# Optimization experiments

Hardware: AMD Instinct MI355X
Metric: run time of the kernel (lower is better)

The kernel has to match this reference:

```python
import jax, jax.numpy as jnp
import numpy as np

N, E, G = 2048, 4096, 16
IN_DIM, HID, E_DIM, EDGE_H = 11, 128, 6, 64
EPS = 1e-5


def setup_inputs() -> dict:
    key = jax.random.key(0)
    ks = jax.random.split(key, 32)
    s = 0.1  # keep activations tame
    inp = {
        "h": jax.random.normal(ks[0], (N, IN_DIM), jnp.float32),
        "e": jax.random.normal(ks[1], (E, E_DIM), jnp.float32),
        "src": jax.random.randint(ks[2], (E,), 0, N, jnp.int32),
        "dst": jax.random.randint(ks[3], (E,), 0, N, jnp.int32),
        "node_graph": (jnp.arange(N, dtype=jnp.int32) // (N // G)),
        # layer 0 (in_dim=11 -> hid=128)
        "eW1_0": jax.random.normal(ks[4], (E_DIM, EDGE_H), jnp.float32) * s,
        "eb1_0": jax.random.normal(ks[5], (EDGE_H,), jnp.float32) * s,
        "eW2_0": jax.random.normal(ks[6], (EDGE_H, IN_DIM * HID), jnp.float32) * s,
        "eb2_0": jax.random.normal(ks[7], (IN_DIM * HID,), jnp.float32) * s,
        "bias_0": jax.random.normal(ks[8], (HID,), jnp.float32) * s,
        "gamma_0": jax.random.uniform(ks[9], (HID,), jnp.float32, 0.5, 1.5),
        "beta_0": jax.random.normal(ks[10], (HID,), jnp.float32) * s,
        "mean_0": jax.random.normal(ks[11], (HID,), jnp.float32) * s,
        "var_0": jax.random.uniform(ks[12], (HID,), jnp.float32, 0.5, 1.5),
        # layers 1..3 stacked (hid -> hid)
        "eW1": jax.random.normal(ks[13], (3, E_DIM, EDGE_H), jnp.float32) * s,
        "eb1": jax.random.normal(ks[14], (3, EDGE_H), jnp.float32) * s,
        "eW2": jax.random.normal(ks[15], (3, EDGE_H, HID * HID), jnp.float32) * s,
        "eb2": jax.random.normal(ks[16], (3, HID * HID), jnp.float32) * s,
        "bias": jax.random.normal(ks[17], (3, HID), jnp.float32) * s,
        "gamma": jax.random.uniform(ks[18], (3, HID), jnp.float32, 0.5, 1.5),
        "beta": jax.random.normal(ks[19], (3, HID), jnp.float32) * s,
        "mean": jax.random.normal(ks[20], (3, HID), jnp.float32) * s,
        "var": jax.random.uniform(ks[21], (3, HID), jnp.float32, 0.5, 1.5),
        # output BN (on mean readout)
        "g_out": jax.random.uniform(ks[22], (HID,), jnp.float32, 0.5, 1.5),
        "b_out": jax.random.normal(ks[23], (HID,), jnp.float32) * s,
        "m_out": jax.random.normal(ks[24], (HID,), jnp.float32) * s,
        "v_out": jax.random.uniform(ks[25], (HID,), jnp.float32, 0.5, 1.5),
    }
    return inp


def _bn(x, ga, be, mu, vv):
    return (x - mu) * jax.lax.rsqrt(vv + EPS) * ga + be


def _nn_layer(x, e, src, dst, W1, b1, W2, b2, bb, ga, be, mu, vv, din):
    # edge MLP -> per-edge weight matrix [E, din, HID]
    w = (jax.nn.relu(e @ W1 + b1) @ W2 + b2).reshape(E, din, HID)
    msg = jnp.einsum('ei,eio->eo', x[src], w)          # per-edge message [E, HID]
    agg = jax.ops.segment_sum(msg, dst, num_segments=N)
    deg = jax.ops.segment_sum(jnp.ones((E,), x.dtype), dst, num_segments=N)
    agg = agg / jnp.maximum(deg, 1.0)[:, None] + bb    # mean aggregation + NNConv bias
    return _bn(jax.nn.relu(agg), ga, be, mu, vv)       # relu -> BatchNorm (eval)


def reference(h, e, src, dst, node_graph, eW1_0, eb1_0, eW2_0, eb2_0, bias_0,
              gamma_0, beta_0, mean_0, var_0, eW1, eb1, eW2, eb2, bias,
              gamma, beta, mean, var, g_out, b_out, m_out, v_out):
    x = _nn_layer(h, e, src, dst, eW1_0, eb1_0, eW2_0, eb2_0, bias_0,
                  gamma_0, beta_0, mean_0, var_0, IN_DIM)
    for i in range(3):
        x = _nn_layer(x, e, src, dst, eW1[i], eb1[i], eW2[i], eb2[i], bias[i],
                      gamma[i], beta[i], mean[i], var[i], HID)
    # dropout is identity in eval mode
    cnt = jax.ops.segment_sum(jnp.ones((N,), x.dtype), node_graph, num_segments=G)
    hn = jax.ops.segment_sum(x, node_graph, num_segments=G) / cnt[:, None]
    hx = jax.ops.segment_max(x, node_graph, num_segments=G)
    hn = _bn(hn, g_out, b_out, m_out, v_out)
    return jnp.concatenate([hn, hx], axis=1)  # [G, 2*HID]
```

## Files before the change

### kernel.cpp

```cpp
#include <hip/hip_runtime.h>
#include <stdint.h>

#define N_NODES 2048
#define N_EDGES 4096
#define N_GRAPH 16
#define IN_DIM  11
#define HID     128
#define E_DIMF  6
#define EDGE_H  64
#define NSLICE  65
#define ZCOLS   (NSLICE*HID)
#define BN_EPS  1e-5f

typedef __attribute__((ext_vector_type(8))) short short8;
typedef __attribute__((ext_vector_type(4))) float f32x4;

static __device__ __forceinline__ float bf2f(unsigned short u) {
  union { float f; uint32_t i; } x; x.i = ((uint32_t)u) << 16; return x.f;
}
static __device__ __forceinline__ unsigned short f2bf(float f) {
  union { float f; uint32_t i; } x; x.f = f;
  uint32_t i = x.i;
  return (unsigned short)((i + 0x7FFFu + ((i >> 16) & 1u)) >> 16);
}

__global__ void calc_deg_i(const int* __restrict__ dst, int* __restrict__ degi) {
  int e = blockIdx.x * 256 + threadIdx.x;
  if (e < N_EDGES) atomicAdd(&degi[dst[e]], 1);
}

__global__ __launch_bounds__(256) void build_offsets(const int* __restrict__ degi,
                                                     int* __restrict__ roff,
                                                     int* __restrict__ cursor) {
  __shared__ int part[256];
  int t = threadIdx.x;
  int base = t * 8;
  int loc[8];
  int s = 0;
#pragma unroll
  for (int j = 0; j < 8; ++j) { loc[j] = s; s += degi[base + j]; }
  part[t] = s;
  __syncthreads();
  int pre = 0;
  for (int i = 0; i < t; ++i) pre += part[i];
#pragma unroll
  for (int j = 0; j < 8; ++j) {
    int v = pre + loc[j];
    roff[base + j] = v;
    cursor[base + j] = v;
  }
  if (t == 255) roff[N_NODES] = pre + s;
}

__global__ void scatter_edges(const int* __restrict__ dst, int* __restrict__ cursor,
                              int* __restrict__ elist) {
  int e = blockIdx.x * 256 + threadIdx.x;
  if (e < N_EDGES) {
    int pos = atomicAdd(&cursor[dst[e]], 1);
    elist[pos] = e;
  }
}

__global__ __launch_bounds__(256) void prep(const float* __restrict__ W2_0,
                                            const float* __restrict__ b2_0,
                                            const float* __restrict__ W2L,
                                            const float* __restrict__ b2L,
                                            const float* __restrict__ h_in,
                                            unsigned short* __restrict__ WbT0,
                                            unsigned short* __restrict__ WbTL,
                                            unsigned short* __restrict__ xb0) {
  const int y = blockIdx.y, t = threadIdx.x;
  if (y == 4) {
    for (int idx = blockIdx.x * 256 + t; idx < N_NODES * 32; idx += 65 * 256) {
      int n = idx >> 5, i = idx & 31;
      xb0[idx] = f2bf(i < IN_DIM ? h_in[n * IN_DIM + i] : 0.0f);
    }
    return;
  }
  __shared__ unsigned short tile[128 * 130];
  const int k = blockIdx.x;
  if (y == 0) {
    const float* src = (k < 64) ? (W2_0 + (size_t)k * IN_DIM * HID) : b2_0;
    for (int j = t; j < IN_DIM * HID; j += 256) {
      int i = j >> 7, o = j & 127;
      tile[i * 130 + o] = f2bf(src[j]);
    }
    __syncthreads();
    for (int j = t; j < HID * 32; j += 256) {
      int o = j >> 5, i = j & 31;
      WbT0[((size_t)k * HID + o) * 32 + i] =
          (i < IN_DIM) ? tile[i * 130 + o] : (unsigned short)0;
    }
  } else {
    const int l = y - 1;
    const float* src = (k < 64) ? (W2L + ((size_t)l * 64 + k) * (HID * HID))
                                : (b2L + (size_t)l * (HID * HID));
    unsigned short* dstp = WbTL + (size_t)l * ZCOLS * HID;
    for (int j = t; j < HID * HID; j += 256) {
      int i = j >> 7, o = j & 127;
      tile[i * 130 + o] = f2bf(src[j]);
    }
    __syncthreads();
    for (int j = t; j < HID * HID; j += 256) {
      int o = j >> 7, i = j & 127;
      dstp[((size_t)k * HID + o) * HID + i] = tile[i * 130 + o];
    }
  }
}

template <int KP, int SWZ>
__global__ __launch_bounds__(256) void gemm_z(const unsigned short* __restrict__ Xb,
                                              const unsigned short* __restrict__ WbT,
                                              unsigned short* __restrict__ Z) {
  extern __shared__ unsigned short lds[];
  unsigned short* Al = lds;
  unsigned short* Bl = lds + 128 * KP;
  const int nb = blockIdx.x;
  const int mb = blockIdx.y;
  const int t = threadIdx.x;
  const int ROWB = KP * 2;
  const int NCH = 128 * ROWB / 16;
  const unsigned short* Asrc = Xb + (size_t)mb * 128 * KP;
  const unsigned short* Bsrc = WbT + (size_t)nb * 128 * KP;
  for (int c = t; c < NCH; c += 256) {
    int off = c * 16;
    int row = off / ROWB;
    int kb = off % ROWB;
    int dsto = row * ROWB + (kb ^ ((row & SWZ) << 4));
    *(uint4*)((char*)Al + dsto) = *(const uint4*)((const char*)Asrc + off);
    *(uint4*)((char*)Bl + dsto) = *(const uint4*)((const char*)Bsrc + off);
  }
  __syncthreads();

  const int w = t >> 6, l = t & 63;
  const int wm = (w >> 1) * 64, wn = (w & 1) * 64;
  const int lr = l & 15, lh = l >> 4;
  f32x4 acc[4][4] = {};
#pragma unroll
  for (int kk = 0; kk < KP; kk += 32) {
    short8 a[4], b[4];
    const int kb = (kk + lh * 8) * 2;
#pragma unroll
    for (int mi = 0; mi < 4; ++mi) {
      int row = wm + mi * 16 + lr;
      int addr = row * ROWB + (kb ^ ((row & SWZ) << 4));
      a[mi] = *(const short8*)((const char*)Al + addr);
    }
#pragma unroll
    for (int ni = 0; ni < 4; ++ni) {
      int col = wn + ni * 16 + lr;
      int addr = col * ROWB + (kb ^ ((col & SWZ) << 4));
      b[ni] = *(const short8*)((const char*)Bl + addr);
    }
#pragma unroll
    for (int mi = 0; mi < 4; ++mi)
#pragma unroll
      for (int ni = 0; ni < 4; ++ni)
        acc[mi][ni] = __builtin_amdgcn_mfma_f32_16x16x32_bf16(b[ni], a[mi], acc[mi][ni], 0, 0, 0);
  }
#pragma unroll
  for (int mi = 0; mi < 4; ++mi) {
    const int node = mb * 128 + wm + mi * 16 + lr;
    unsigned short* zp = Z + (size_t)node * ZCOLS + nb * 128 + wn + lh * 4;
#pragma unroll
    for (int ni = 0; ni < 4; ++ni) {
      ushort4 pk;
      pk.x = f2bf(acc[mi][ni][0]);
      pk.y = f2bf(acc[mi][ni][1]);
      pk.z = f2bf(acc[mi][ni][2]);
      pk.w = f2bf(acc[mi][ni][3]);
      *(ushort4*)(zp + ni * 16) = pk;
    }
  }
}

template <int LAST>
__global__ __launch_bounds__(128) void node_gather(
    const float* __restrict__ efeat, const float* __restrict__ W1,
    const float* __restrict__ b1, const unsigned short* __restrict__ Z,
    const int* __restrict__ elist, const int* __restrict__ roff,
    const int* __restrict__ src,
    const float* __restrict__ bias, const float* __restrict__ gamma,
    const float* __restrict__ beta, const float* __restrict__ mean,
    const float* __restrict__ var,
    unsigned short* __restrict__ xbout,
    const int* __restrict__ ng, float* __restrict__ gsum,
    unsigned int* __restrict__ gmax, float* __restrict__ gcnt) {
  const int n = blockIdx.x, t = threadIdx.x;
  const int cg = t & 15, kg = t >> 4;
  const int start = roff[n], end = roff[n + 1];
  __shared__ float hs[EDGE_H];
  __shared__ float red[128][9];
  float acc8[8] = {};
  for (int idx = start; idx < end; ++idx) {
    const int e = elist[idx];
    __syncthreads();
    if (t < EDGE_H) {
      float a = b1[t];
#pragma unroll
      for (int j = 0; j < E_DIMF; ++j) a += efeat[e * E_DIMF + j] * W1[j * EDGE_H + t];
      hs[t] = fmaxf(a, 0.f);
    }
    __syncthreads();
    const unsigned short* zr = Z + (size_t)src[e] * ZCOLS + cg * 8;
#pragma unroll
    for (int kk = 0; kk < 8; ++kk) {
      const int k = kg * 8 + kk;
      short8 v = *(const short8*)(zr + k * HID);
      const float hk = hs[k];
#pragma unroll
      for (int j = 0; j < 8; ++j) acc8[j] += hk * bf2f((unsigned short)v[j]);
    }
    if (kg == 0) {
      short8 v = *(const short8*)(zr + 64 * HID);
#pragma unroll
      for (int j = 0; j < 8; ++j) acc8[j] += bf2f((unsigned short)v[j]);
    }
  }
#pragma unroll
  for (int j = 0; j < 8; ++j) red[t][j] = acc8[j];
  __syncthreads();
  const int o = t;
  float s = 0.f;
#pragma unroll
  for (int k2 = 0; k2 < 8; ++k2) s += red[k2 * 16 + (o >> 3)][o & 7];
  const int dg = end - start;
  float v = s / (float)(dg > 0 ? dg : 1) + bias[o];
  v = fmaxf(v, 0.f);
  v = (v - mean[o]) * rsqrtf(var[o] + BN_EPS) * gamma[o] + beta[o];
  if (!LAST) {
    xbout[n * HID + o] = f2bf(v);
  } else {
    const int g = ng[n];
    atomicAdd(&gsum[g * HID + o], v);
    unsigned int u = __float_as_uint(v);
    unsigned int key = (u & 0x80000000u) ? ~u : (u | 0x80000000u);
    atomicMax(&gmax[g * HID + o], key);
    if (o == 0) atomicAdd(&gcnt[g], 1.f);
  }
}

__global__ void out_final(const float* __restrict__ gsum, const unsigned int* __restrict__ gmax,
                          const float* __restrict__ gcnt,
                          const float* __restrict__ g_out, const float* __restrict__ b_out,
                          const float* __restrict__ m_out, const float* __restrict__ v_out,
                          float* __restrict__ out) {
  int g = blockIdx.x, t = threadIdx.x;
  float hn = gsum[g * HID + t] / fmaxf(gcnt[g], 1.0f);
  hn = (hn - m_out[t]) * rsqrtf(v_out[t] + BN_EPS) * g_out[t] + b_out[t];
  unsigned int key = gmax[g * HID + t];
  unsigned int u = (key & 0x80000000u) ? (key ^ 0x80000000u) : ~key;
  out[g * 2 * HID + t] = hn;
  out[g * 2 * HID + HID + t] = __uint_as_float(u);
}

extern "C" void kernel_launch(void* const* d_in, const int* in_sizes, int n_in,
                              void* d_out, int out_size, void* d_ws, size_t ws_size,
                              hipStream_t stream) {
  const float* h_in   = (const float*)d_in[0];
  const float* e_in   = (const float*)d_in[1];
  const int*   src    = (const int*)d_in[2];
  const int*   dst    = (const int*)d_in[3];
  const int*   ng     = (const int*)d_in[4];
  const float* eW1_0  = (const float*)d_in[5];
  const float* eb1_0  = (const float*)d_in[6];
  const float* eW2_0  = (const float*)d_in[7];
  const float* eb2_0  = (const float*)d_in[8];
  const float* bias_0 = (const float*)d_in[9];
  const float* gamma_0= (const float*)d_in[10];
  const float* beta_0 = (const float*)d_in[11];
  const float* mean_0 = (const float*)d_in[12];
  const float* var_0  = (const float*)d_in[13];
  const float* eW1    = (const float*)d_in[14];
  const float* eb1    = (const float*)d_in[15];
  const float* eW2    = (const float*)d_in[16];
  const float* eb2    = (const float*)d_in[17];
  const float* biasL  = (const float*)d_in[18];
  const float* gammaL = (const float*)d_in[19];
  const float* betaL  = (const float*)d_in[20];
  const float* meanL  = (const float*)d_in[21];
  const float* varL   = (const float*)d_in[22];
  const float* g_out  = (const float*)d_in[23];
  const float* b_out  = (const float*)d_in[24];
  const float* m_out  = (const float*)d_in[25];
  const float* v_out  = (const float*)d_in[26];
  float* out = (float*)d_out;

  char* ws = (char*)d_ws;
  size_t off = 0;
  auto alloc = [&](size_t bytes) {
    void* p = ws + off;
    off = (off + bytes + 255) & ~(size_t)255;
    return p;
  };
  unsigned short* Z    = (unsigned short*)alloc((size_t)N_NODES * ZCOLS * 2);
  unsigned short* WbT0 = (unsigned short*)alloc((size_t)ZCOLS * 32 * 2);
  unsigned short* WbTL = (unsigned short*)alloc((size_t)3 * ZCOLS * HID * 2);
  unsigned short* xb0  = (unsigned short*)alloc((size_t)N_NODES * 32 * 2);
  unsigned short* xb   = (unsigned short*)alloc((size_t)N_NODES * HID * 2);
  float* gsum          = (float*)alloc((size_t)N_GRAPH * HID * 4);
  unsigned int* gmax   = (unsigned int*)alloc((size_t)N_GRAPH * HID * 4);
  float* gcnt          = (float*)alloc((size_t)N_GRAPH * 4);
  int*   degi          = (int*)alloc((size_t)N_NODES * 4);
  size_t zbytes = (size_t)((char*)(degi + N_NODES) - (char*)gsum);
  int* roff            = (int*)alloc((size_t)(N_NODES + 1) * 4);
  int* cursor          = (int*)alloc((size_t)N_NODES * 4);
  int* elist           = (int*)alloc((size_t)N_EDGES * 4);

  hipMemsetAsync(gsum, 0, zbytes, stream);
  calc_deg_i<<<N_EDGES / 256, 256, 0, stream>>>(dst, degi);
  build_offsets<<<1, 256, 0, stream>>>(degi, roff, cursor);
  scatter_edges<<<N_EDGES / 256, 256, 0, stream>>>(dst, cursor, elist);
  prep<<<dim3(65, 5), 256, 0, stream>>>(eW2_0, eb2_0, eW2, eb2, h_in, WbT0, WbTL, xb0);

  gemm_z<32, 3><<<dim3(65, 16), 256, 2 * 128 * 32 * 2, stream>>>(xb0, WbT0, Z);
  node_gather<0><<<N_NODES, 128, 0, stream>>>(e_in, eW1_0, eb1_0, Z, elist, roff, src,
                                              bias_0, gamma_0, beta_0, mean_0, var_0,
                                              xb, ng, gsum, gmax, gcnt);

  for (int l = 0; l < 3; ++l) {
    gemm_z<128, 7><<<dim3(65, 16), 256, 2 * 128 * 128 * 2, stream>>>(
        xb, WbTL + (size_t)l * ZCOLS * HID, Z);
    if (l < 2) {
      node_gather<0><<<N_NODES, 128, 0, stream>>>(
          e_in, eW1 + l * E_DIMF * EDGE_H, eb1 + l * EDGE_H, Z, elist, roff, src,
          biasL + l * HID, gammaL + l * HID, betaL + l * HID, meanL + l * HID,
          varL + l * HID, xb, ng, gsum, gmax, gcnt);
    } else {
      node_gather<1><<<N_NODES, 128, 0, stream>>>(
          e_in, eW1 + l * E_DIMF * EDGE_H, eb1 + l * EDGE_H, Z, elist, roff, src,
          biasL + l * HID, gammaL + l * HID, betaL + l * HID, meanL + l * HID,
          varL + l * HID, xb, ng, gsum, gmax, gcnt);
    }
  }

  out_final<<<N_GRAPH, HID, 0, stream>>>(gsum, gmax, gcnt, g_out, b_out, m_out, v_out, out);
}
```

Baseline: 203.0 us.

## Fuse whole pipeline into one cooperative persistent kernel with grid syncs

Replaces the sequence of about a dozen launches (degree count, offsets, scatter, weight transpose, GEMMs, gathers, readout) with one cooperative kernel of 256 blocks by 512 threads that separates phases with grid-wide syncs. It also reworks the gather so each block handles four nodes at once and every thread computes the edge MLP hidden values itself, removing the per-edge LDS broadcast and its block barriers. The aim is to cut launch overhead and inter-kernel gaps. In exchange, the GEMM and transpose now run as persistent loops on a fixed grid, which may lower occupancy and parallelism, and every phase boundary pays a grid barrier. The old multi-launch path stays as a fallback when cooperative launch is unavailable.

```diff
diff --git a/kernel.cpp b/kernel.cpp
--- a/kernel.cpp
+++ b/kernel.cpp
@@ -1,5 +1,8 @@
 #include <hip/hip_runtime.h>
+#include <hip/hip_cooperative_groups.h>
 #include <stdint.h>
+
+namespace cg = cooperative_groups;
 
 #define N_NODES 2048
 #define N_EDGES 4096
@@ -11,6 +14,8 @@
 #define NSLICE  65
 #define ZCOLS   (NSLICE*HID)
 #define BN_EPS  1e-5f
+#define MEGA_BLOCKS 256
+#define MEGA_THREADS 512
 
 typedef __attribute__((ext_vector_type(8))) short short8;
 typedef __attribute__((ext_vector_type(4))) float f32x4;
@@ -23,6 +28,286 @@
   uint32_t i = x.i;
   return (unsigned short)((i + 0x7FFFu + ((i >> 16) & 1u)) >> 16);
 }
+
+struct MegaP {
+  const float *h_in, *e_in;
+  const int *src, *dst, *ng;
+  const float *eW1_0, *eb1_0, *eW2_0, *eb2_0;
+  const float *bias_0, *gamma_0, *beta_0, *mean_0, *var_0;
+  const float *eW1, *eb1, *eW2, *eb2;
+  const float *biasL, *gammaL, *betaL, *meanL, *varL;
+  const float *g_out, *b_out, *m_out, *v_out;
+  float *out;
+  unsigned short *Z, *WbT0, *WbTL, *xb0, *xb;
+  float *gsum;
+  unsigned int *gmax;
+  float *gcnt;
+  int *roff, *cursor, *elist;
+};
+
+
+static __device__ void transpose_slab(const MegaP& p, int s, char* smem) {
+  unsigned short* tile = (unsigned short*)smem;
+  const int t = threadIdx.x;
+  if (s < 65) {
+    const int k = s;
+    const float* srcp = (k < 64) ? (p.eW2_0 + (size_t)k * IN_DIM * HID) : p.eb2_0;
+    for (int j = t; j < IN_DIM * HID; j += MEGA_THREADS) {
+      int i = j >> 7, o = j & 127;
+      tile[i * 130 + o] = f2bf(srcp[j]);
+    }
+    __syncthreads();
+    for (int j = t; j < HID * 32; j += MEGA_THREADS) {
+      int o = j >> 5, i = j & 31;
+      p.WbT0[((size_t)k * HID + o) * 32 + i] =
+          (i < IN_DIM) ? tile[i * 130 + o] : (unsigned short)0;
+    }
+    __syncthreads();
+  } else {
+    const int sl = s - 65, l = sl / 65, k = sl % 65;
+    const float* srcp = (k < 64) ? (p.eW2 + ((size_t)l * 64 + k) * (HID * HID))
+                                 : (p.eb2 + (size_t)l * (HID * HID));
+    unsigned short* dstp = p.WbTL + (size_t)l * ZCOLS * HID;
+    for (int j = t; j < HID * HID; j += MEGA_THREADS) {
+      int i = j >> 7, o = j & 127;
+      tile[i * 130 + o] = f2bf(srcp[j]);
+    }
+    __syncthreads();
+    for (int j = t; j < HID * HID; j += MEGA_THREADS) {
+      int o = j >> 7, i = j & 127;
+      dstp[((size_t)k * HID + o) * HID + i] = tile[i * 130 + o];
+    }
+    __syncthreads();
+  }
+}
+
+template <int KP, int SWZ>
+static __device__ void gemm_phase(const unsigned short* Xb, const unsigned short* WbT,
+                                  unsigned short* Z, char* smem) {
+  unsigned short* Al = (unsigned short*)smem;
+  unsigned short* Bl = Al + 128 * KP;
+  const int t = threadIdx.x;
+  const int ROWB = KP * 2;
+  const int NCH = 128 * ROWB / 16;
+  const int w = t >> 6, l = t & 63;
+  const int wm = (w >> 2) * 64, wn = (w & 3) * 32;
+  const int lr = l & 15, lh = l >> 4;
+  for (int tile = blockIdx.x; tile < 65 * 16; tile += gridDim.x) {
+    const int nb = tile % 65, mb = tile / 65;
+    const unsigned short* Asrc = Xb + (size_t)mb * 128 * KP;
+    const unsigned short* Bsrc = WbT + (size_t)nb * 128 * KP;
+    for (int c = t; c < NCH; c += MEGA_THREADS) {
+      int off = c * 16;
+      int row = off / ROWB;
+      int kb = off % ROWB;
+      int dsto = row * ROWB + (kb ^ ((row & SWZ) << 4));
+      *(uint4*)((char*)Al + dsto) = *(const uint4*)((const char*)Asrc + off);
+      *(uint4*)((char*)Bl + dsto) = *(const uint4*)((const char*)Bsrc + off);
+    }
+    __syncthreads();
+    f32x4 acc[4][2] = {};
+#pragma unroll
+    for (int kk = 0; kk < KP; kk += 32) {
+      short8 a[4], b[2];
+      const int kb = (kk + lh * 8) * 2;
+#pragma unroll
+      for (int mi = 0; mi < 4; ++mi) {
+        int row = wm + mi * 16 + lr;
+        int addr = row * ROWB + (kb ^ ((row & SWZ) << 4));
+        a[mi] = *(const short8*)((const char*)Al + addr);
+      }
+#pragma unroll
+      for (int ni = 0; ni < 2; ++ni) {
+        int col = wn + ni * 16 + lr;
+        int addr = col * ROWB + (kb ^ ((col & SWZ) << 4));
+        b[ni] = *(const short8*)((const char*)Bl + addr);
+      }
+#pragma unroll
+      for (int mi = 0; mi < 4; ++mi)
+#pragma unroll
+        for (int ni = 0; ni < 2; ++ni)
+          acc[mi][ni] = __builtin_amdgcn_mfma_f32_16x16x32_bf16(b[ni], a[mi], acc[mi][ni], 0, 0, 0);
+    }
+#pragma unroll
+    for (int mi = 0; mi < 4; ++mi) {
+      const int node = mb * 128 + wm + mi * 16 + lr;
+      unsigned short* zp = Z + (size_t)node * ZCOLS + nb * 128 + wn + lh * 4;
+#pragma unroll
+      for (int ni = 0; ni < 2; ++ni) {
+        ushort4 pk;
+        pk.x = f2bf(acc[mi][ni][0]);
+        pk.y = f2bf(acc[mi][ni][1]);
+        pk.z = f2bf(acc[mi][ni][2]);
+        pk.w = f2bf(acc[mi][ni][3]);
+        *(ushort4*)(zp + ni * 16) = pk;
+      }
+    }
+    __syncthreads();
+  }
+}
+
+template <int LAST>
+static __device__ void gather_phase(const MegaP& p, const float* W1, const float* b1,
+                                    const float* bias, const float* gamma,
+                                    const float* beta, const float* mean,
+                                    const float* var, char* smem) {
+  float* red = (float*)smem;
+  const int t = threadIdx.x;
+  const int hh = t >> 7, tt = t & 127;
+  const int cgi = tt & 15, kg = tt >> 4;
+  for (int n0 = blockIdx.x * 4; n0 < N_NODES; n0 += gridDim.x * 4) {
+    const int n = n0 + hh;
+    const int start = p.roff[n], end = p.roff[n + 1];
+    float acc8[8] = {};
+    for (int idx = start; idx < end; ++idx) {
+      const int e = p.elist[idx];
+      float ef[E_DIMF];
+#pragma unroll
+      for (int j = 0; j < E_DIMF; ++j) ef[j] = p.e_in[e * E_DIMF + j];
+      float hk[8];
+#pragma unroll
+      for (int kk = 0; kk < 8; ++kk) {
+        const int k = kg * 8 + kk;
+        float a = b1[k];
+#pragma unroll
+        for (int j = 0; j < E_DIMF; ++j) a += ef[j] * W1[j * EDGE_H + k];
+        hk[kk] = fmaxf(a, 0.f);
+      }
+      const unsigned short* zr = p.Z + (size_t)p.src[e] * ZCOLS + cgi * 8;
+#pragma unroll
+      for (int kk = 0; kk < 8; ++kk) {
+        short8 v = *(const short8*)(zr + (kg * 8 + kk) * HID);
+        const float hv = hk[kk];
+#pragma unroll
+        for (int j = 0; j < 8; ++j) acc8[j] += hv * bf2f((unsigned short)v[j]);
+      }
+      if (kg == 0) {
+        short8 v = *(const short8*)(zr + 64 * HID);
+#pragma unroll
+        for (int j = 0; j < 8; ++j) acc8[j] += bf2f((unsigned short)v[j]);
+      }
+    }
+    __syncthreads();
+#pragma unroll
+    for (int j = 0; j < 8; ++j) red[(hh * 128 + tt) * 9 + j] = acc8[j];
+    __syncthreads();
+    const int o = tt;
+    float s = 0.f;
+#pragma unroll
+    for (int k2 = 0; k2 < 8; ++k2) s += red[(hh * 128 + k2 * 16 + (o >> 3)) * 9 + (o & 7)];
+    const int dg = end - start;
+    float v = s / (float)(dg > 0 ? dg : 1) + bias[o];
+    v = fmaxf(v, 0.f);
+    v = (v - mean[o]) * rsqrtf(var[o] + BN_EPS) * gamma[o] + beta[o];
+    if (!LAST) {
+      p.xb[n * HID + o] = f2bf(v);
+    } else {
+      const int g = p.ng[n];
+      atomicAdd(&p.gsum[g * HID + o], v);
+      unsigned int u = __float_as_uint(v);
+      unsigned int key = (u & 0x80000000u) ? ~u : (u | 0x80000000u);
+      atomicMax(&p.gmax[g * HID + o], key);
+      if (o == 0) atomicAdd(&p.gcnt[g], 1.f);
+    }
+  }
+}
+
+static __device__ __forceinline__ void gsync(cg::grid_group& g) {
+  __threadfence();
+  g.sync();
+  __threadfence();
+}
+
+__global__ __launch_bounds__(MEGA_THREADS, 2) void mega(MegaP p) {
+  cg::grid_group grid = cg::this_grid();
+  extern __shared__ char smem[];
+  const int bid = blockIdx.x, t = threadIdx.x;
+  const int NB = gridDim.x;
+
+  for (int i = bid * MEGA_THREADS + t; i < N_GRAPH * HID; i += NB * MEGA_THREADS) {
+    p.gsum[i] = 0.f;
+    p.gmax[i] = 0u;
+  }
+  if (bid == 1 && t < N_GRAPH) p.gcnt[t] = 0.f;
+  for (int idx = bid * MEGA_THREADS + t; idx < N_NODES * 32; idx += NB * MEGA_THREADS) {
+    int n = idx >> 5, i = idx & 31;
+    p.xb0[idx] = f2bf(i < IN_DIM ? p.h_in[n * IN_DIM + i] : 0.f);
+  }
+  if (bid == 0) {
+    int* hist = (int*)smem;
+    int* part = hist + N_NODES;
+    for (int i = t; i < N_NODES; i += MEGA_THREADS) hist[i] = 0;
+    __syncthreads();
+    for (int e = t; e < N_EDGES; e += MEGA_THREADS) atomicAdd(&hist[p.dst[e]], 1);
+    __syncthreads();
+    if (t < 256) {
+      const int base = t * 8;
+      int s = 0;
+#pragma unroll
+      for (int j = 0; j < 8; ++j) s += hist[base + j];
+      part[t] = s;
+    }
+    __syncthreads();
+    for (int d = 1; d < 256; d <<= 1) {
+      int v = 0;
+      if (t < 256) { v = part[t]; if (t >= d) v += part[t - d]; }
+      __syncthreads();
+      if (t < 256) part[t] = v;
+      __syncthreads();
+    }
+    if (t < 256) {
+      const int pre = (t == 0) ? 0 : part[t - 1];
+      const int base = t * 8;
+      int s = 0;
+#pragma unroll
+      for (int j = 0; j < 8; ++j) {
+        p.roff[base + j] = pre + s;
+        p.cursor[base + j] = pre + s;
+        s += hist[base + j];
+      }
+      if (t == 255) p.roff[N_NODES] = pre + s;
+    }
+  } else {
+    for (int s = bid - 1; s < 260; s += NB - 1) transpose_slab(p, s, smem);
+  }
+  gsync(grid);
+
+  for (int e = bid * MEGA_THREADS + t; e < N_EDGES; e += NB * MEGA_THREADS) {
+    const int pos = atomicAdd(&p.cursor[p.dst[e]], 1);
+    p.elist[pos] = e;
+  }
+  gemm_phase<32, 3>(p.xb0, p.WbT0, p.Z, smem);
+  gsync(grid);
+
+  gather_phase<0>(p, p.eW1_0, p.eb1_0, p.bias_0, p.gamma_0, p.beta_0,
+                  p.mean_0, p.var_0, smem);
+  gsync(grid);
+
+  for (int l = 0; l < 3; ++l) {
+    gemm_phase<128, 7>(p.xb, p.WbTL + (size_t)l * ZCOLS * HID, p.Z, smem);
+    gsync(grid);
+    const float* W1 = p.eW1 + l * E_DIMF * EDGE_H;
+    const float* b1 = p.eb1 + l * EDGE_H;
+    if (l < 2)
+      gather_phase<0>(p, W1, b1, p.biasL + l * HID, p.gammaL + l * HID,
+                      p.betaL + l * HID, p.meanL + l * HID, p.varL + l * HID, smem);
+    else
+      gather_phase<1>(p, W1, b1, p.biasL + l * HID, p.gammaL + l * HID,
+                      p.betaL + l * HID, p.meanL + l * HID, p.varL + l * HID, smem);
+    gsync(grid);
+  }
+
+  if (bid < 4) {
+    const int g = bid * 4 + (t >> 7), o = t & 127;
+    float hn = p.gsum[g * HID + o] / fmaxf(p.gcnt[g], 1.f);
+    hn = (hn - p.m_out[o]) * rsqrtf(p.v_out[o] + BN_EPS) * p.g_out[o] + p.b_out[o];
+    const unsigned int key = p.gmax[g * HID + o];
+    const unsigned int u = (key & 0x80000000u) ? (key ^ 0x80000000u) : ~key;
+    p.out[g * 2 * HID + o] = hn;
+    p.out[g * 2 * HID + HID + o] = __uint_as_float(u);
+  }
+}
+
 
 __global__ void calc_deg_i(const int* __restrict__ dst, int* __restrict__ degi) {
   int e = blockIdx.x * 256 + threadIdx.x;
@@ -131,7 +416,6 @@
     *(uint4*)((char*)Bl + dsto) = *(const uint4*)((const char*)Bsrc + off);
   }
   __syncthreads();
-
   const int w = t >> 6, l = t & 63;
   const int wm = (w >> 1) * 64, wn = (w & 1) * 64;
   const int lr = l & 15, lh = l >> 4;
@@ -187,7 +471,7 @@
     const int* __restrict__ ng, float* __restrict__ gsum,
     unsigned int* __restrict__ gmax, float* __restrict__ gcnt) {
   const int n = blockIdx.x, t = threadIdx.x;
-  const int cg = t & 15, kg = t >> 4;
+  const int cg2 = t & 15, kg = t >> 4;
   const int start = roff[n], end = roff[n + 1];
   __shared__ float hs[EDGE_H];
   __shared__ float red[128][9];
@@ -202,7 +486,7 @@
       hs[t] = fmaxf(a, 0.f);
     }
     __syncthreads();
-    const unsigned short* zr = Z + (size_t)src[e] * ZCOLS + cg * 8;
+    const unsigned short* zr = Z + (size_t)src[e] * ZCOLS + cg2 * 8;
 #pragma unroll
     for (int kk = 0; kk < 8; ++kk) {
       const int k = kg * 8 + kk;
@@ -254,85 +538,104 @@
   out[g * 2 * HID + HID + t] = __uint_as_float(u);
 }
 
+
 extern "C" void kernel_launch(void* const* d_in, const int* in_sizes, int n_in,
                               void* d_out, int out_size, void* d_ws, size_t ws_size,
                               hipStream_t stream) {
-  const float* h_in   = (const float*)d_in[0];
-  const float* e_in   = (const float*)d_in[1];
-  const int*   src    = (const int*)d_in[2];
-  const int*   dst    = (const int*)d_in[3];
-  const int*   ng     = (const int*)d_in[4];
-  const float* eW1_0  = (const float*)d_in[5];
-  const float* eb1_0  = (const float*)d_in[6];
-  const float* eW2_0  = (const float*)d_in[7];
-  const float* eb2_0  = (const float*)d_in[8];
-  const float* bias_0 = (const float*)d_in[9];
-  const float* gamma_0= (const float*)d_in[10];
-  const float* beta_0 = (const float*)d_in[11];
-  const float* mean_0 = (const float*)d_in[12];
-  const float* var_0  = (const float*)d_in[13];
-  const float* eW1    = (const float*)d_in[14];
-  const float* eb1    = (const float*)d_in[15];
-  const float* eW2    = (const float*)d_in[16];
-  const float* eb2    = (const float*)d_in[17];
-  const float* biasL  = (const float*)d_in[18];
-  const float* gammaL = (const float*)d_in[19];
-  const float* betaL  = (const float*)d_in[20];
-  const float* meanL  = (const float*)d_in[21];
-  const float* varL   = (const float*)d_in[22];
-  const float* g_out  = (const float*)d_in[23];
-  const float* b_out  = (const float*)d_in[24];
-  const float* m_out  = (const float*)d_in[25];
-  const float* v_out  = (const float*)d_in[26];
-  float* out = (float*)d_out;
-
   char* ws = (char*)d_ws;
   size_t off = 0;
   auto alloc = [&](size_t bytes) {
-    void* p = ws + off;
+    void* pp = ws + off;
     off = (off + bytes + 255) & ~(size_t)255;
-    return p;
+    return pp;
   };
-  unsigned short* Z    = (unsigned short*)alloc((size_t)N_NODES * ZCOLS * 2);
-  unsigned short* WbT0 = (unsigned short*)alloc((size_t)ZCOLS * 32 * 2);
-  unsigned short* WbTL = (unsigned short*)alloc((size_t)3 * ZCOLS * HID * 2);
-  unsigned short* xb0  = (unsigned short*)alloc((size_t)N_NODES * 32 * 2);
-  unsigned short* xb   = (unsigned short*)alloc((size_t)N_NODES * HID * 2);
-  float* gsum          = (float*)alloc((size_t)N_GRAPH * HID * 4);
-  unsigned int* gmax   = (unsigned int*)alloc((size_t)N_GRAPH * HID * 4);
-  float* gcnt          = (float*)alloc((size_t)N_GRAPH * 4);
-  int*   degi          = (int*)alloc((size_t)N_NODES * 4);
-  size_t zbytes = (size_t)((char*)(degi + N_NODES) - (char*)gsum);
-  int* roff            = (int*)alloc((size_t)(N_NODES + 1) * 4);
-  int* cursor          = (int*)alloc((size_t)N_NODES * 4);
-  int* elist           = (int*)alloc((size_t)N_EDGES * 4);
-
-  hipMemsetAsync(gsum, 0, zbytes, stream);
-  calc_deg_i<<<N_EDGES / 256, 256, 0, stream>>>(dst, degi);
-  build_offsets<<<1, 256, 0, stream>>>(degi, roff, cursor);
-  scatter_edges<<<N_EDGES / 256, 256, 0, stream>>>(dst, cursor, elist);
-  prep<<<dim3(65, 5), 256, 0, stream>>>(eW2_0, eb2_0, eW2, eb2, h_in, WbT0, WbTL, xb0);
-
-  gemm_z<32, 3><<<dim3(65, 16), 256, 2 * 128 * 32 * 2, stream>>>(xb0, WbT0, Z);
-  node_gather<0><<<N_NODES, 128, 0, stream>>>(e_in, eW1_0, eb1_0, Z, elist, roff, src,
-                                              bias_0, gamma_0, beta_0, mean_0, var_0,
-                                              xb, ng, gsum, gmax, gcnt);
-
+
+  MegaP P;
+  P.h_in    = (const float*)d_in[0];
+  P.e_in    = (const float*)d_in[1];
+  P.src     = (const int*)d_in[2];
+  P.dst     = (const int*)d_in[3];
+  P.ng      = (const int*)d_in[4];
+  P.eW1_0   = (const float*)d_in[5];
+  P.eb1_0   = (const float*)d_in[6];
+  P.eW2_0   = (const float*)d_in[7];
+  P.eb2_0   = (const float*)d_in[8];
+  P.bias_0  = (const float*)d_in[9];
+  P.gamma_0 = (const float*)d_in[10];
+  P.beta_0  = (const float*)d_in[11];
+  P.mean_0  = (const float*)d_in[12];
+  P.var_0   = (const float*)d_in[13];
+  P.eW1     = (const float*)d_in[14];
+  P.eb1     = (const float*)d_in[15];
+  P.eW2     = (const float*)d_in[16];
+  P.eb2     = (const float*)d_in[17];
+  P.biasL   = (const float*)d_in[18];
+  P.gammaL  = (const float*)d_in[19];
+  P.betaL   = (const float*)d_in[20];
+  P.meanL   = (const float*)d_in[21];
+  P.varL    = (const float*)d_in[22];
+  P.g_out   = (const float*)d_in[23];
+  P.b_out   = (const float*)d_in[24];
+  P.m_out   = (const float*)d_in[25];
+  P.v_out   = (const float*)d_in[26];
+  P.out     = (float*)d_out;
+
+  P.Z     = (unsigned short*)alloc((size_t)N_NODES * ZCOLS * 2);
+  P.WbT0  = (unsigned short*)alloc((size_t)ZCOLS * 32 * 2);
+  P.WbTL  = (unsigned short*)alloc((size_t)3 * ZCOLS * HID * 2);
+  P.xb0   = (unsigned short*)alloc((size_t)N_NODES * 32 * 2);
+  P.xb    = (unsigned short*)alloc((size_t)N_NODES * HID * 2);
+  P.gsum  = (float*)alloc((size_t)N_GRAPH * HID * 4);
+  P.gmax  = (unsigned int*)alloc((size_t)N_GRAPH * HID * 4);
+  P.gcnt  = (float*)alloc((size_t)N_GRAPH * 4);
+  int* degi = (int*)alloc((size_t)N_NODES * 4);
+  P.roff  = (int*)alloc((size_t)(N_NODES + 1) * 4);
+  P.cursor= (int*)alloc((size_t)N_NODES * 4);
+  P.elist = (int*)alloc((size_t)N_EDGES * 4);
+
+  int dev = 0;
+  hipGetDevice(&dev);
+  int coopAttr = 0;
+  hipDeviceGetAttribute(&coopAttr, hipDeviceAttributeCooperativeLaunch, dev);
+  int maxBlk = 0;
+  hipError_t occErr = hipOccupancyMaxActiveBlocksPerMultiprocessor(
+      &maxBlk, (const void*)mega, MEGA_THREADS, 65536);
+  bool useCoop = (coopAttr != 0) && (occErr == hipSuccess) && (maxBlk >= 1);
+
+  if (useCoop) {
+    void* args[] = {(void*)&P};
+    hipError_t lerr = hipLaunchCooperativeKernel((const void*)mega, dim3(MEGA_BLOCKS),
+                                                 dim3(MEGA_THREADS), args, 65536, stream);
+    if (lerr == hipSuccess) return;
+  }
+
+  hipMemsetAsync(P.gsum, 0,
+                 (size_t)((char*)(degi + N_NODES) - (char*)P.gsum), stream);
+  calc_deg_i<<<N_EDGES / 256, 256, 0, stream>>>(P.dst, degi);
+  build_offsets<<<1, 256, 0, stream>>>(degi, P.roff, P.cursor);
+  scatter_edges<<<N_EDGES / 256, 256, 0, stream>>>(P.dst, P.cursor, P.elist);
+  prep<<<dim3(65, 5), 256, 0, stream>>>(P.eW2_0, P.eb2_0, P.eW2, P.eb2, P.h_in,
+                                        P.WbT0, P.WbTL, P.xb0);
+
+  gemm_z<32, 3><<<dim3(65, 16), 256, 2 * 128 * 32 * 2, stream>>>(P.xb0, P.WbT0, P.Z);
+  node_gather<0><<<N_NODES, 128, 0, stream>>>(P.e_in, P.eW1_0, P.eb1_0, P.Z, P.elist,
+                                              P.roff, P.src, P.bias_0, P.gamma_0,
+                                              P.beta_0, P.mean_0, P.var_0, P.xb,
+                                              P.ng, P.gsum, P.gmax, P.gcnt);
   for (int l = 0; l < 3; ++l) {
     gemm_z<128, 7><<<dim3(65, 16), 256, 2 * 128 * 128 * 2, stream>>>(
-        xb, WbTL + (size_t)l * ZCOLS * HID, Z);
-    if (l < 2) {
+        P.xb, P.WbTL + (size_t)l * ZCOLS * HID, P.Z);
+    if (l < 2)
       node_gather<0><<<N_NODES, 128, 0, stream>>>(
-          e_in, eW1 + l * E_DIMF * EDGE_H, eb1 + l * EDGE_H, Z, elist, roff, src,
-          biasL + l * HID, gammaL + l * HID, betaL + l * HID, meanL + l * HID,
-          varL + l * HID, xb, ng, gsum, gmax, gcnt);
-    } else {
+          P.e_in, P.eW1 + l * E_DIMF * EDGE_H, P.eb1 + l * EDGE_H, P.Z, P.elist,
+          P.roff, P.src, P.biasL + l * HID, P.gammaL + l * HID, P.betaL + l * HID,
+          P.meanL + l * HID, P.varL + l * HID, P.xb, P.ng, P.gsum, P.gmax, P.gcnt);
+    else
       node_gather<1><<<N_NODES, 128, 0, stream>>>(
-          e_in, eW1 + l * E_DIMF * EDGE_H, eb1 + l * EDGE_H, Z, elist, roff, src,
-          biasL + l * HID, gammaL + l * HID, betaL + l * HID, meanL + l * HID,
-          varL + l * HID, xb, ng, gsum, gmax, gcnt);
-    }
-  }
-
-  out_final<<<N_GRAPH, HID, 0, stream>>>(gsum, gmax, gcnt, g_out, b_out, m_out, v_out, out);
-}
+          P.e_in, P.eW1 + l * E_DIMF * EDGE_H, P.eb1 + l * EDGE_H, P.Z, P.elist,
+          P.roff, P.src, P.biasL + l * HID, P.gammaL + l * HID, P.betaL + l * HID,
+          P.meanL + l * HID, P.varL + l * HID, P.xb, P.ng, P.gsum, P.gmax, P.gcnt);
+  }
+  out_final<<<N_GRAPH, HID, 0, stream>>>(P.gsum, P.gmax, P.gcnt, P.g_out, P.b_out,
+                                         P.m_out, P.v_out, P.out);
+}
```

After: 199.9 us. About the same (-1.5%).

## Fuse CSR build and prep into one kernel; fold final readout into last gather

Applied to the files above, without the earlier changes.

Replaces the memset, degree count, offset scan, edge scatter and weight-prep launches with a single prep_all kernel. One block builds the CSR in shared memory while the other blocks convert weights and zero the accumulators. The out_final kernel is removed: the last node_gather block to finish, detected with an atomic done counter, computes the readout BN and the max. This cuts about five launches and their gaps, but the CSR build now runs serially in one block and the readout in one block.

```diff
diff --git a/kernel.cpp b/kernel.cpp
--- a/kernel.cpp
+++ b/kernel.cpp
@@ -24,87 +24,98 @@
   return (unsigned short)((i + 0x7FFFu + ((i >> 16) & 1u)) >> 16);
 }
 
-__global__ void calc_deg_i(const int* __restrict__ dst, int* __restrict__ degi) {
-  int e = blockIdx.x * 256 + threadIdx.x;
-  if (e < N_EDGES) atomicAdd(&degi[dst[e]], 1);
-}
-
-__global__ __launch_bounds__(256) void build_offsets(const int* __restrict__ degi,
-                                                     int* __restrict__ roff,
-                                                     int* __restrict__ cursor) {
-  __shared__ int part[256];
-  int t = threadIdx.x;
-  int base = t * 8;
-  int loc[8];
-  int s = 0;
-#pragma unroll
-  for (int j = 0; j < 8; ++j) { loc[j] = s; s += degi[base + j]; }
-  part[t] = s;
-  __syncthreads();
-  int pre = 0;
-  for (int i = 0; i < t; ++i) pre += part[i];
-#pragma unroll
-  for (int j = 0; j < 8; ++j) {
-    int v = pre + loc[j];
-    roff[base + j] = v;
-    cursor[base + j] = v;
-  }
-  if (t == 255) roff[N_NODES] = pre + s;
-}
-
-__global__ void scatter_edges(const int* __restrict__ dst, int* __restrict__ cursor,
-                              int* __restrict__ elist) {
-  int e = blockIdx.x * 256 + threadIdx.x;
-  if (e < N_EDGES) {
-    int pos = atomicAdd(&cursor[dst[e]], 1);
-    elist[pos] = e;
-  }
-}
-
-__global__ __launch_bounds__(256) void prep(const float* __restrict__ W2_0,
-                                            const float* __restrict__ b2_0,
-                                            const float* __restrict__ W2L,
-                                            const float* __restrict__ b2L,
-                                            const float* __restrict__ h_in,
-                                            unsigned short* __restrict__ WbT0,
-                                            unsigned short* __restrict__ WbTL,
-                                            unsigned short* __restrict__ xb0) {
-  const int y = blockIdx.y, t = threadIdx.x;
-  if (y == 4) {
-    for (int idx = blockIdx.x * 256 + t; idx < N_NODES * 32; idx += 65 * 256) {
+struct PrepP {
+  const float *eW2_0, *eb2_0, *eW2, *eb2, *h_in;
+  const int *dst;
+  unsigned short *WbT0, *WbTL, *xb0;
+  int *roff, *elist;
+  float *gsum;
+  unsigned int *gmax;
+  float *gcnt;
+  int *donecnt;
+};
+
+#define PREP_BLOCKS 271
+__global__ __launch_bounds__(256) void prep_all(PrepP p) {
+  const int bid = blockIdx.x, t = threadIdx.x;
+  __shared__ union {
+    struct { int hist[N_NODES]; int part[256]; } csr;
+    unsigned short tile[128 * 130];
+  } sm;
+
+  if (bid == 0) {
+    for (int i = t; i < N_NODES; i += 256) sm.csr.hist[i] = 0;
+    __syncthreads();
+    for (int e = t; e < N_EDGES; e += 256) atomicAdd(&sm.csr.hist[p.dst[e]], 1);
+    __syncthreads();
+    const int base = t * 8;
+    int loc[8];
+    int s = 0;
+#pragma unroll
+    for (int j = 0; j < 8; ++j) { loc[j] = s; s += sm.csr.hist[base + j]; }
+    sm.csr.part[t] = s;
+    __syncthreads();
+    for (int d = 1; d < 256; d <<= 1) {
+      int v = sm.csr.part[t];
+      if (t >= d) v += sm.csr.part[t - d];
+      __syncthreads();
+      sm.csr.part[t] = v;
+      __syncthreads();
+    }
+    const int pre = (t == 0) ? 0 : sm.csr.part[t - 1];
+#pragma unroll
+    for (int j = 0; j < 8; ++j) p.roff[base + j] = pre + loc[j];
+    if (t == 255) p.roff[N_NODES] = pre + s;
+    __syncthreads();
+#pragma unroll
+    for (int j = 0; j < 8; ++j) sm.csr.hist[base + j] = pre + loc[j];
+    __syncthreads();
+    for (int e = t; e < N_EDGES; e += 256) {
+      int pos = atomicAdd(&sm.csr.hist[p.dst[e]], 1);
+      p.elist[pos] = e;
+    }
+  } else if (bid <= 260) {
+    const int s = bid - 1;
+    if (s < 65) {
+      const int k = s;
+      const float* srcp = (k < 64) ? (p.eW2_0 + (size_t)k * IN_DIM * HID) : p.eb2_0;
+      for (int j = t; j < IN_DIM * HID; j += 256) {
+        int i = j >> 7, o = j & 127;
+        sm.tile[i * 130 + o] = f2bf(srcp[j]);
+      }
+      __syncthreads();
+      for (int j = t; j < HID * 32; j += 256) {
+        int o = j >> 5, i = j & 31;
+        p.WbT0[((size_t)k * HID + o) * 32 + i] =
+            (i < IN_DIM) ? sm.tile[i * 130 + o] : (unsigned short)0;
+      }
+    } else {
+      const int sl = s - 65, l = sl / 65, k = sl % 65;
+      const float* srcp = (k < 64) ? (p.eW2 + ((size_t)l * 64 + k) * (HID * HID))
+                                   : (p.eb2 + (size_t)l * (HID * HID));
+      unsigned short* dstp = p.WbTL + (size_t)l * ZCOLS * HID;
+      for (int j = t; j < HID * HID; j += 256) {
+        int i = j >> 7, o = j & 127;
+        sm.tile[i * 130 + o] = f2bf(srcp[j]);
+      }
+      __syncthreads();
+      for (int j = t; j < HID * HID; j += 256) {
+        int o = j >> 7, i = j & 127;
+        dstp[((size_t)k * HID + o) * HID + i] = sm.tile[i * 130 + o];
+      }
+    }
+  } else if (bid <= 268) {
+    for (int idx = (bid - 261) * 256 + t; idx < N_NODES * 32; idx += 8 * 256) {
       int n = idx >> 5, i = idx & 31;
-      xb0[idx] = f2bf(i < IN_DIM ? h_in[n * IN_DIM + i] : 0.0f);
-    }
-    return;
-  }
-  __shared__ unsigned short tile[128 * 130];
-  const int k = blockIdx.x;
-  if (y == 0) {
-    const float* src = (k < 64) ? (W2_0 + (size_t)k * IN_DIM * HID) : b2_0;
-    for (int j = t; j < IN_DIM * HID; j += 256) {
-      int i = j >> 7, o = j & 127;
-      tile[i * 130 + o] = f2bf(src[j]);
-    }
-    __syncthreads();
-    for (int j = t; j < HID * 32; j += 256) {
-      int o = j >> 5, i = j & 31;
-      WbT0[((size_t)k * HID + o) * 32 + i] =
-          (i < IN_DIM) ? tile[i * 130 + o] : (unsigned short)0;
+      p.xb0[idx] = f2bf(i < IN_DIM ? p.h_in[n * IN_DIM + i] : 0.f);
     }
   } else {
-    const int l = y - 1;
-    const float* src = (k < 64) ? (W2L + ((size_t)l * 64 + k) * (HID * HID))
-                                : (b2L + (size_t)l * (HID * HID));
-    unsigned short* dstp = WbTL + (size_t)l * ZCOLS * HID;
-    for (int j = t; j < HID * HID; j += 256) {
-      int i = j >> 7, o = j & 127;
-      tile[i * 130 + o] = f2bf(src[j]);
-    }
-    __syncthreads();
-    for (int j = t; j < HID * HID; j += 256) {
-      int o = j >> 7, i = j & 127;
-      dstp[((size_t)k * HID + o) * HID + i] = tile[i * 130 + o];
-    }
+    for (int i = (bid - 269) * 256 + t; i < N_GRAPH * HID; i += 2 * 256) {
+      p.gsum[i] = 0.f;
+      p.gmax[i] = 0u;
+    }
+    if (bid == 269 && t < N_GRAPH) p.gcnt[t] = 0.f;
+    if (bid == 270 && t == 0) *p.donecnt = 0;
   }
 }
 
@@ -131,7 +142,6 @@
     *(uint4*)((char*)Bl + dsto) = *(const uint4*)((const char*)Bsrc + off);
   }
   __syncthreads();
-
   const int w = t >> 6, l = t & 63;
   const int wm = (w >> 1) * 64, wn = (w & 1) * 64;
   const int lr = l & 15, lh = l >> 4;
@@ -185,9 +195,13 @@
     const float* __restrict__ var,
     unsigned short* __restrict__ xbout,
     const int* __restrict__ ng, float* __restrict__ gsum,
-    unsigned int* __restrict__ gmax, float* __restrict__ gcnt) {
+    unsigned int* __restrict__ gmax, float* __restrict__ gcnt,
+    int* __restrict__ donecnt,
+    const float* __restrict__ g_out, const float* __restrict__ b_out,
+    const float* __restrict__ m_out, const float* __restrict__ v_out,
+    float* __restrict__ out) {
   const int n = blockIdx.x, t = threadIdx.x;
-  const int cg = t & 15, kg = t >> 4;
+  const int cg2 = t & 15, kg = t >> 4;
   const int start = roff[n], end = roff[n + 1];
   __shared__ float hs[EDGE_H];
   __shared__ float red[128][9];
@@ -202,7 +216,7 @@
       hs[t] = fmaxf(a, 0.f);
     }
     __syncthreads();
-    const unsigned short* zr = Z + (size_t)src[e] * ZCOLS + cg * 8;
+    const unsigned short* zr = Z + (size_t)src[e] * ZCOLS + cg2 * 8;
 #pragma unroll
     for (int kk = 0; kk < 8; ++kk) {
       const int k = kg * 8 + kk;
@@ -237,22 +251,27 @@
     unsigned int key = (u & 0x80000000u) ? ~u : (u | 0x80000000u);
     atomicMax(&gmax[g * HID + o], key);
     if (o == 0) atomicAdd(&gcnt[g], 1.f);
-  }
-}
-
-__global__ void out_final(const float* __restrict__ gsum, const unsigned int* __restrict__ gmax,
-                          const float* __restrict__ gcnt,
-                          const float* __restrict__ g_out, const float* __restrict__ b_out,
-                          const float* __restrict__ m_out, const float* __restrict__ v_out,
-                          float* __restrict__ out) {
-  int g = blockIdx.x, t = threadIdx.x;
-  float hn = gsum[g * HID + t] / fmaxf(gcnt[g], 1.0f);
-  hn = (hn - m_out[t]) * rsqrtf(v_out[t] + BN_EPS) * g_out[t] + b_out[t];
-  unsigned int key = gmax[g * HID + t];
-  unsigned int u = (key & 0x80000000u) ? (key ^ 0x80000000u) : ~key;
-  out[g * 2 * HID + t] = hn;
-  out[g * 2 * HID + HID + t] = __uint_as_float(u);
-}
+    __threadfence();
+    __shared__ int lastFlag;
+    if (t == 0) lastFlag = (atomicAdd(donecnt, 1) == N_NODES - 1);
+    __syncthreads();
+    if (lastFlag) {
+      __threadfence();
+      for (int i = t; i < N_GRAPH * HID; i += 128) {
+        const int gg = i >> 7, oo = i & 127;
+        float sum = atomicAdd(&gsum[i], 0.f);
+        float cnt = atomicAdd(&gcnt[gg], 0.f);
+        unsigned int key2 = atomicOr(&gmax[i], 0u);
+        float hn = sum / fmaxf(cnt, 1.f);
+        hn = (hn - m_out[oo]) * rsqrtf(v_out[oo] + BN_EPS) * g_out[oo] + b_out[oo];
+        const unsigned int uu = (key2 & 0x80000000u) ? (key2 ^ 0x80000000u) : ~key2;
+        out[gg * 2 * HID + oo] = hn;
+        out[gg * 2 * HID + HID + oo] = __uint_as_float(uu);
+      }
+    }
+  }
+}
+
 
 extern "C" void kernel_launch(void* const* d_in, const int* in_sizes, int n_in,
                               void* d_out, int out_size, void* d_ws, size_t ws_size,
@@ -289,9 +308,9 @@
   char* ws = (char*)d_ws;
   size_t off = 0;
   auto alloc = [&](size_t bytes) {
-    void* p = ws + off;
+    void* pp = ws + off;
     off = (off + bytes + 255) & ~(size_t)255;
-    return p;
+    return pp;
   };
   unsigned short* Z    = (unsigned short*)alloc((size_t)N_NODES * ZCOLS * 2);
   unsigned short* WbT0 = (unsigned short*)alloc((size_t)ZCOLS * 32 * 2);
@@ -301,38 +320,39 @@
   float* gsum          = (float*)alloc((size_t)N_GRAPH * HID * 4);
   unsigned int* gmax   = (unsigned int*)alloc((size_t)N_GRAPH * HID * 4);
   float* gcnt          = (float*)alloc((size_t)N_GRAPH * 4);
-  int*   degi          = (int*)alloc((size_t)N_NODES * 4);
-  size_t zbytes = (size_t)((char*)(degi + N_NODES) - (char*)gsum);
+  int* donecnt         = (int*)alloc(256);
   int* roff            = (int*)alloc((size_t)(N_NODES + 1) * 4);
-  int* cursor          = (int*)alloc((size_t)N_NODES * 4);
   int* elist           = (int*)alloc((size_t)N_EDGES * 4);
 
-  hipMemsetAsync(gsum, 0, zbytes, stream);
-  calc_deg_i<<<N_EDGES / 256, 256, 0, stream>>>(dst, degi);
-  build_offsets<<<1, 256, 0, stream>>>(degi, roff, cursor);
-  scatter_edges<<<N_EDGES / 256, 256, 0, stream>>>(dst, cursor, elist);
-  prep<<<dim3(65, 5), 256, 0, stream>>>(eW2_0, eb2_0, eW2, eb2, h_in, WbT0, WbTL, xb0);
+  PrepP P;
+  P.eW2_0 = eW2_0; P.eb2_0 = eb2_0; P.eW2 = eW2; P.eb2 = eb2; P.h_in = h_in;
+  P.dst = dst;
+  P.WbT0 = WbT0; P.WbTL = WbTL; P.xb0 = xb0;
+  P.roff = roff; P.elist = elist;
+  P.gsum = gsum; P.gmax = gmax; P.gcnt = gcnt; P.donecnt = donecnt;
+
+  prep_all<<<PREP_BLOCKS, 256, 0, stream>>>(P);
 
   gemm_z<32, 3><<<dim3(65, 16), 256, 2 * 128 * 32 * 2, stream>>>(xb0, WbT0, Z);
   node_gather<0><<<N_NODES, 128, 0, stream>>>(e_in, eW1_0, eb1_0, Z, elist, roff, src,
                                               bias_0, gamma_0, beta_0, mean_0, var_0,
-                                              xb, ng, gsum, gmax, gcnt);
+                                              xb, ng, gsum, gmax, gcnt, donecnt,
+                                              g_out, b_out, m_out, v_out, out);
 
   for (int l = 0; l < 3; ++l) {
     gemm_z<128, 7><<<dim3(65, 16), 256, 2 * 128 * 128 * 2, stream>>>(
         xb, WbTL + (size_t)l * ZCOLS * HID, Z);
-    if (l < 2) {
+    if (l < 2)
       node_gather<0><<<N_NODES, 128, 0, stream>>>(
           e_in, eW1 + l * E_DIMF * EDGE_H, eb1 + l * EDGE_H, Z, elist, roff, src,
           biasL + l * HID, gammaL + l * HID, betaL + l * HID, meanL + l * HID,
-          varL + l * HID, xb, ng, gsum, gmax, gcnt);
-    } else {
+          varL + l * HID, xb, ng, gsum, gmax, gcnt, donecnt,
+          g_out, b_out, m_out, v_out, out);
+    else
       node_gather<1><<<N_NODES, 128, 0, stream>>>(
           e_in, eW1 + l * E_DIMF * EDGE_H, eb1 + l * EDGE_H, Z, elist, roff, src,
           biasL + l * HID, gammaL + l * HID, betaL + l * HID, meanL + l * HID,
-          varL + l * HID, xb, ng, gsum, gmax, gcnt);
-    }
-  }
-
-  out_final<<<N_GRAPH, HID, 0, stream>>>(gsum, gmax, gcnt, g_out, b_out, m_out, v_out, out);
-}
+          varL + l * HID, xb, ng, gsum, gmax, gcnt, donecnt,
+          g_out, b_out, m_out, v_out, out);
+  }
+}
```

Result: slower. 362.8 us (+78.7%).
